# Kernel tuning notes

Measured on AMD Instinct MI355X. Metric: run time of the kernel, lower is better.

The kernel has to match this reference:

```python
import jax, jax.numpy as jnp
import numpy as np

N, D, H, K, E = 50000, 128, 4, 20, 1600000
DH = D // H
EPS = 1e-5

def _ln(x, g, b):
    m = x.mean(-1, keepdims=True)
    v = x.var(-1, keepdims=True)
    return (x - m) / jnp.sqrt(v + EPS) * g + b

def _mha(q_in, kv, in_w, in_b, out_w, out_b):
    # q_in: [N,1,D], kv: [N,K,D]; PyTorch nn.MultiheadAttention math (eval mode)
    wq, wk, wv = jnp.split(in_w, 3, axis=0)
    bq, bk, bv = jnp.split(in_b, 3, axis=0)
    n, kk, _ = kv.shape
    q = (q_in @ wq.T + bq).reshape(n, 1, H, DH)
    k = (kv @ wk.T + bk).reshape(n, kk, H, DH)
    v = (kv @ wv.T + bv).reshape(n, kk, H, DH)
    s = jnp.einsum('nqhd,nkhd->nhqk', q, k) / jnp.sqrt(jnp.asarray(DH, q.dtype))
    a = jax.nn.softmax(s, axis=-1)
    o = jnp.einsum('nhqk,nkhd->nqhd', a, v).reshape(n, 1, D)
    return o @ out_w.T + out_b

def setup_inputs() -> dict:
    key = jax.random.key(0)
    ks = jax.random.split(key, 12)
    s = 0.02
    return {
        'x': jax.random.normal(ks[0], (N, D), jnp.float32),
        'attention_samples': jax.random.randint(ks[1], (N, K), 0, N),
        'edge_src': jax.random.randint(ks[2], (E,), 0, N),
        'edge_dst': jax.random.randint(ks[3], (E,), 0, N),
        't_in_w': jax.random.normal(ks[4], (3, 3 * D, D), jnp.float32) * s,
        't_in_b': jnp.zeros((3, 3 * D), jnp.float32),
        't_out_w': jax.random.normal(ks[5], (3, D, D), jnp.float32) * s,
        't_out_b': jnp.zeros((3, D), jnp.float32),
        't_ffn_w1': jax.random.normal(ks[6], (3, 4 * D, D), jnp.float32) * s,
        't_ffn_b1': jnp.zeros((3, 4 * D), jnp.float32),
        't_ffn_w2': jax.random.normal(ks[7], (3, D, 4 * D), jnp.float32) * s,
        't_ffn_b2': jnp.zeros((3, D), jnp.float32),
        't_ln1_g': jnp.ones((3, D), jnp.float32),
        't_ln1_b': jnp.zeros((3, D), jnp.float32),
        't_ln2_g': jnp.ones((3, D), jnp.float32),
        't_ln2_b': jnp.zeros((3, D), jnp.float32),
        'g_w': jax.random.normal(ks[8], (2, D, 2 * D), jnp.float32) * s,
        'g_b': jnp.zeros((2, D), jnp.float32),
        'g_ln_g': jnp.ones((2, D), jnp.float32),
        'g_ln_b': jnp.zeros((2, D), jnp.float32),
    }

def reference(x, attention_samples, edge_src, edge_dst,
              t_in_w, t_in_b, t_out_w, t_out_b,
              t_ffn_w1, t_ffn_b1, t_ffn_w2, t_ffn_b2,
              t_ln1_g, t_ln1_b, t_ln2_g, t_ln2_b,
              g_w, g_b, g_ln_g, g_ln_b):
    def trans(h, i):
        kv = h[attention_samples]                      # [N,K,D] irregular gather
        attn = _mha(h[:, None, :], kv, t_in_w[i], t_in_b[i], t_out_w[i], t_out_b[i])[:, 0, :]
        h = _ln(h + attn, t_ln1_g[i], t_ln1_b[i])
        f = jax.nn.relu(h @ t_ffn_w1[i].T + t_ffn_b1[i]) @ t_ffn_w2[i].T + t_ffn_b2[i]
        return _ln(h + f, t_ln2_g[i], t_ln2_b[i])
    def gnn(h, i):
        neigh = jax.ops.segment_sum(h[edge_dst], edge_src, num_segments=N)  # spmm(adj, h)
        comb = jnp.concatenate([h, neigh], axis=-1)
        hn = jax.nn.relu(comb @ g_w[i].T + g_b[i])
        return _ln(hn + h, g_ln_g[i], g_ln_b[i])
    # Trans1 -> GNN1 -> Trans2 -> GNN2 -> Trans3
    x = trans(x, 0)
    x = gnn(x, 0)
    x = trans(x, 1)
    x = gnn(x, 1)
    x = trans(x, 2)
    return x
```

## Files before the change

kernel.cpp:

```cpp
#include <hip/hip_runtime.h>

#define DM 128
#define KS 20
#define BW 512
#define BSH 9
#define MAXB 128
#define HP 264

typedef __attribute__((ext_vector_type(8))) short short8;
typedef __attribute__((ext_vector_type(4))) float f32x4;
typedef __attribute__((ext_vector_type(2))) float f32x2;
typedef __attribute__((ext_vector_type(2))) __bf16 bf16x2;

__device__ __forceinline__ unsigned short f2b(float f) {
    unsigned u = __float_as_uint(f);
    u += 0x7fff + ((u >> 16) & 1);
    return (unsigned short)(u >> 16);
}
__device__ __forceinline__ float b2f(unsigned short b) {
    return __uint_as_float(((unsigned)b) << 16);
}
__device__ __forceinline__ float blo(unsigned u) { return __uint_as_float(u << 16); }
__device__ __forceinline__ float bhi(unsigned u) { return __uint_as_float(u & 0xffff0000u); }
__device__ __forceinline__ unsigned pk(float a, float b) {
    return (unsigned)f2b(a) | ((unsigned)f2b(b) << 16);
}

#if __has_builtin(__builtin_amdgcn_fdot2_f32_bf16)
__device__ __forceinline__ float dot2bf(unsigned a, unsigned b, float acc) {
    return __builtin_amdgcn_fdot2_f32_bf16(
        __builtin_bit_cast(bf16x2, a), __builtin_bit_cast(bf16x2, b), acc, false);
}
#else
__device__ __forceinline__ float dot2bf(unsigned a, unsigned b, float acc) {
    return acc + blo(a) * blo(b) + bhi(a) * bhi(b);
}
#endif

__device__ __forceinline__ float f8dec_sw(unsigned char b) {
    const int s = b >> 7, e = (b >> 3) & 15, m = b & 7;
    float v = e ? ldexpf((float)(8 + m), e - 10) : ldexpf((float)m, -9);
    return s ? -v : v;
}
template <bool HI>
__device__ __forceinline__ f32x2 fp8x2(unsigned u) {
#if __has_builtin(__builtin_amdgcn_cvt_pk_f32_fp8)
    return __builtin_amdgcn_cvt_pk_f32_fp8(u, HI);
#else
    const unsigned w = HI ? (u >> 16) : (u & 0xffffu);
    return (f32x2){f8dec_sw((unsigned char)(w & 0xff)),
                   f8dec_sw((unsigned char)(w >> 8))};
#endif
}
__device__ __forceinline__ unsigned char f8enc(float v) {
#if __has_builtin(__builtin_amdgcn_cvt_pk_fp8_f32)
    return (unsigned char)(__builtin_amdgcn_cvt_pk_fp8_f32(v, v, 0, false) & 0xff);
#else
    unsigned u = __float_as_uint(v);
    unsigned s = (u >> 24) & 0x80;
    unsigned a = u & 0x7fffffffu;
    if (a >= 0x43e00000u) return (unsigned char)(s | 0x7e);
    if (a < 0x3c000000u) {
        int r = (int)(__uint_as_float(a) * 512.f + 0.5f);
        if (r > 7) return (unsigned char)(s | 0x08);
        return (unsigned char)(s | (unsigned)r);
    }
    unsigned r = a + 0x7ffffu + ((a >> 20) & 1);
    unsigned e = (r >> 23) - 120;
    unsigned m = (r >> 20) & 7;
    return (unsigned char)(s | (e << 3) | m);
#endif
}

__global__ __launch_bounds__(256) void xcvt_kernel(
    const float* __restrict__ x, float* __restrict__ h,
    unsigned short* __restrict__ hb, int n)
{
    const int i = (blockIdx.x * 256 + threadIdx.x) * 4;
    if (i < n) {
        const float4 v = *(const float4*)(x + i);
        *(float4*)(h + i) = v;
        ((unsigned*)hb)[i / 2]     = pk(v.x, v.y);
        ((unsigned*)hb)[i / 2 + 1] = pk(v.z, v.w);
    }
}

__global__ __launch_bounds__(256) void setup_kernel(
    const float* __restrict__ t_in_w,  const float* __restrict__ t_out_w,
    const float* __restrict__ t_ffn_w1, const float* __restrict__ t_ffn_w2,
    const float* __restrict__ g_w, unsigned short* __restrict__ wbuf,
    unsigned* __restrict__ WoP, int* __restrict__ bcnt)
{
    const int tid = blockIdx.x * 256 + threadIdx.x;
    if (tid < 163840) {
        const int i4 = tid * 4;
        const float* src; int rel;
        if      (i4 < 147456) { src = t_in_w;   rel = i4; }
        else if (i4 < 196608) { src = t_out_w;  rel = i4 - 147456; }
        else if (i4 < 393216) { src = t_ffn_w1; rel = i4 - 196608; }
        else if (i4 < 589824) { src = t_ffn_w2; rel = i4 - 393216; }
        else                  { src = g_w;      rel = i4 - 589824; }
        const float4 v = *(const float4*)(src + rel);
        ((unsigned*)wbuf)[i4 / 2]     = pk(v.x, v.y);
        ((unsigned*)wbuf)[i4 / 2 + 1] = pk(v.z, v.w);
    } else if (tid < 163840 + 24576) {
        const int t2 = tid - 163840;
        const int i = t2 / 8192, rem = t2 % 8192;
        const int plane = rem >> 12, r2 = rem & 4095;
        const int k2 = r2 >> 6, j = r2 & 63;
        const int col = j + plane * 64;
        const float* W = t_out_w + (size_t)i * 16384;
        WoP[(size_t)i * 8192 + plane * 4096 + k2 * 64 + j] =
            pk(W[col * 128 + 2 * k2], W[col * 128 + 2 * k2 + 1]);
    } else if (tid < 163840 + 24576 + MAXB) {
        bcnt[tid - 163840 - 24576] = 0;
    }
}

__global__ __launch_bounds__(256) void gemm_qkv(
    const unsigned short* __restrict__ X,
    const unsigned short* __restrict__ W, const float* __restrict__ bias,
    unsigned short* __restrict__ Qbf, unsigned char* __restrict__ kv8, int M)
{
    const int tid  = threadIdx.x;
    const int wave = tid >> 6;
    const int lane = tid & 63;
    const int m0 = blockIdx.x * 128 + (wave >> 1) * 64;
    const int c0 = blockIdx.y * 64 + (wave & 1) * 32;
    const int lrow = lane & 15;
    const int quad = lane >> 4;

    f32x4 acc[4][2];
    #pragma unroll
    for (int i = 0; i < 4; ++i)
        #pragma unroll
        for (int j = 0; j < 2; ++j)
            acc[i][j] = (f32x4){0.f, 0.f, 0.f, 0.f};

    int rr[4]; bool vv[4];
    #pragma unroll
    for (int i = 0; i < 4; ++i) { rr[i] = m0 + i * 16 + lrow; vv[i] = rr[i] < M; }

    #pragma unroll
    for (int k0 = 0; k0 < 128; k0 += 32) {
        const int ko = k0 + quad * 8;
        short8 a[4];
        #pragma unroll
        for (int i = 0; i < 4; ++i) {
            a[i] = short8{};
            if (vv[i]) a[i] = *(const short8*)(X + (size_t)rr[i] * 128 + ko);
        }
        const short8 b0 = *(const short8*)(W + (size_t)(c0 + lrow) * 128 + ko);
        const short8 b1 = *(const short8*)(W + (size_t)(c0 + 16 + lrow) * 128 + ko);
        #pragma unroll
        for (int i = 0; i < 4; ++i) {
            acc[i][0] = __builtin_amdgcn_mfma_f32_16x16x32_bf16(a[i], b0, acc[i][0], 0, 0, 0);
            acc[i][1] = __builtin_amdgcn_mfma_f32_16x16x32_bf16(a[i], b1, acc[i][1], 0, 0, 0);
        }
    }

    const bool isQ = (c0 < 128);
    #pragma unroll
    for (int i = 0; i < 4; ++i) {
        const int rb = m0 + i * 16 + quad * 4;
        #pragma unroll
        for (int j = 0; j < 2; ++j) {
            const int col = c0 + j * 16 + lrow;
            const float bsv = bias[col];
            #pragma unroll
            for (int r = 0; r < 4; ++r) {
                const int row = rb + r;
                if (row < M) {
                    const float v = acc[i][j][r] + bsv;
                    if (isQ) Qbf[(size_t)row * 128 + col] = f2b(v);
                    else     kv8[(size_t)row * 256 + (col - 128)] = f8enc(v);
                }
            }
        }
    }
}

template <int CI, bool RELU, int SPLIT>
__global__ __launch_bounds__(256) void gemm_ln(
    const unsigned short* __restrict__ X0, const unsigned short* __restrict__ X1,
    const unsigned short* __restrict__ W, const float* __restrict__ bias,
    const float* __restrict__ resid,
    const float* __restrict__ g, const float* __restrict__ be,
    float* __restrict__ hF, unsigned short* __restrict__ hB, int M)
{
    __shared__ float psum[64][2][2];
    __shared__ float stats[64][2];

    const int tid  = threadIdx.x;
    const int wave = tid >> 6;
    const int lane = tid & 63;
    const int wr = (wave >> 1) * 32;
    const int wc = wave & 1;
    const int m0 = blockIdx.x * 64 + wr;
    const int c0 = wc * 64;
    const int lrow = lane & 15;
    const int quad = lane >> 4;

    f32x4 acc[2][4];
    #pragma unroll
    for (int i = 0; i < 2; ++i)
        #pragma unroll
        for (int j = 0; j < 4; ++j)
            acc[i][j] = (f32x4){0.f, 0.f, 0.f, 0.f};

    const int r0 = m0 + lrow;
    const int r1 = m0 + 16 + lrow;
    const bool v0 = r0 < M, v1 = r1 < M;

    for (int k0 = 0; k0 < CI; k0 += 32) {
        const unsigned short* xs;
        int kk, stride;
        if (SPLIT > 0 && k0 >= SPLIT) { xs = X1; kk = k0 - SPLIT; stride = CI - SPLIT; }
        else                          { xs = X0; kk = k0;         stride = (SPLIT > 0) ? SPLIT : CI; }
        const int ko = kk + quad * 8;
        short8 a0 = {}, a1 = {};
        if (v0) a0 = *(const short8*)(xs + (size_t)r0 * stride + ko);
        if (v1) a1 = *(const short8*)(xs + (size_t)r1 * stride + ko);
        const int kw = k0 + quad * 8;
        #pragma unroll
        for (int j = 0; j < 4; ++j) {
            const short8 bf = *(const short8*)(W + (size_t)(c0 + j * 16 + lrow) * CI + kw);
            acc[0][j] = __builtin_amdgcn_mfma_f32_16x16x32_bf16(a0, bf, acc[0][j], 0, 0, 0);
            acc[1][j] = __builtin_amdgcn_mfma_f32_16x16x32_bf16(a1, bf, acc[1][j], 0, 0, 0);
        }
    }

    float bcol[4], gcol[4], bec[4];
    #pragma unroll
    for (int j = 0; j < 4; ++j) {
        const int col = c0 + j * 16 + lrow;
        bcol[j] = bias[col];
        gcol[j] = g[col];
        bec[j]  = be[col];
    }

    float vals[2][4][4];
    #pragma unroll
    for (int i = 0; i < 2; ++i) {
        #pragma unroll
        for (int r = 0; r < 4; ++r) {
            const int lrel = wr + i * 16 + quad * 4 + r;
            const int row = blockIdx.x * 64 + lrel;
            const bool vr = row < M;
            float s = 0.f, s2 = 0.f;
            #pragma unroll
            for (int j = 0; j < 4; ++j) {
                const int col = c0 + j * 16 + lrow;
                float v = acc[i][j][r] + bcol[j];
                if (RELU) v = fmaxf(v, 0.f);
                if (vr) v += resid[(size_t)row * 128 + col];
                vals[i][j][r] = v;
                s += v; s2 += v * v;
            }
            s  += __shfl_xor(s, 1);  s  += __shfl_xor(s, 2);
            s  += __shfl_xor(s, 4);  s  += __shfl_xor(s, 8);
            s2 += __shfl_xor(s2, 1); s2 += __shfl_xor(s2, 2);
            s2 += __shfl_xor(s2, 4); s2 += __shfl_xor(s2, 8);
            if (lrow == 0) { psum[lrel][wc][0] = s; psum[lrel][wc][1] = s2; }
        }
    }
    __syncthreads();
    if (tid < 64) {
        const float sum   = psum[tid][0][0] + psum[tid][1][0];
        const float sumsq = psum[tid][0][1] + psum[tid][1][1];
        const float mean = sum * (1.f / 128.f);
        const float var  = sumsq * (1.f / 128.f) - mean * mean;
        stats[tid][0] = mean;
        stats[tid][1] = rsqrtf(var + 1e-5f);
    }
    __syncthreads();

    #pragma unroll
    for (int i = 0; i < 2; ++i) {
        #pragma unroll
        for (int r = 0; r < 4; ++r) {
            const int lrel = wr + i * 16 + quad * 4 + r;
            const int row = blockIdx.x * 64 + lrel;
            if (row < M) {
                const float mean = stats[lrel][0];
                const float rstd = stats[lrel][1];
                #pragma unroll
                for (int j = 0; j < 4; ++j) {
                    const int col = c0 + j * 16 + lrow;
                    const float o = (vals[i][j][r] - mean) * rstd * gcol[j] + bec[j];
                    hF[(size_t)row * 128 + col] = o;
                    hB[(size_t)row * 128 + col] = f2b(o);
                }
            }
        }
    }
}

__global__ __launch_bounds__(256, 4) void ffn_fused(
    const unsigned short* __restrict__ X,
    const unsigned short* __restrict__ W1,
    const float* __restrict__ b1,
    const unsigned short* __restrict__ W2,
    const float* __restrict__ b2,
    const float* __restrict__ resid,
    const float* __restrict__ g, const float* __restrict__ be,
    float* __restrict__ hF, unsigned short* __restrict__ hB, int M)
{
    __shared__ unsigned short Hs[32 * HP];
    __shared__ float psum[32][4][2];
    __shared__ float stats[32][2];

    const int tid  = threadIdx.x;
    const int wave = tid >> 6;
    const int lane = tid & 63;
    const int lrow = lane & 15;
    const int quad = lane >> 4;
    const int m0 = blockIdx.x * 32;

    const int c0 = wave * 32;

    const int r0 = m0 + lrow;
    const int r1 = m0 + 16 + lrow;
    const bool v0 = r0 < M, v1 = r1 < M;

    short8 xa[4], xb[4];
    #pragma unroll
    for (int k = 0; k < 4; ++k) {
        const int ko = k * 32 + quad * 8;
        xa[k] = short8{}; xb[k] = short8{};
        if (v0) xa[k] = *(const short8*)(X + (size_t)r0 * 128 + ko);
        if (v1) xb[k] = *(const short8*)(X + (size_t)r1 * 128 + ko);
    }

    float res[2][4][2];
    #pragma unroll
    for (int i = 0; i < 2; ++i)
        #pragma unroll
        for (int r = 0; r < 4; ++r) {
            const int row = m0 + i * 16 + quad * 4 + r;
            const bool vr = row < M;
            #pragma unroll
            for (int j = 0; j < 2; ++j)
                res[i][r][j] = vr ? resid[(size_t)row * 128 + c0 + j * 16 + lrow] : 0.f;
        }

    f32x4 acc2[2][2];
    #pragma unroll
    for (int i = 0; i < 2; ++i)
        #pragma unroll
        for (int j = 0; j < 2; ++j)
            acc2[i][j] = (f32x4){0.f, 0.f, 0.f, 0.f};

    #pragma unroll
    for (int chunk = 0; chunk < 2; ++chunk) {
        const int cb = chunk * 256 + wave * 64;
        const int lcb = wave * 64;
        {
            f32x4 acc[2][4];
            #pragma unroll
            for (int i = 0; i < 2; ++i)
                #pragma unroll
                for (int j = 0; j < 4; ++j)
                    acc[i][j] = (f32x4){0.f, 0.f, 0.f, 0.f};

            #pragma unroll
            for (int k = 0; k < 4; ++k) {
                const int ko = k * 32 + quad * 8;
                #pragma unroll
                for (int j = 0; j < 4; ++j) {
                    const short8 bf = *(const short8*)(W1 + (size_t)(cb + j * 16 + lrow) * 128 + ko);
                    acc[0][j] = __builtin_amdgcn_mfma_f32_16x16x32_bf16(xa[k], bf, acc[0][j], 0, 0, 0);
                    acc[1][j] = __builtin_amdgcn_mfma_f32_16x16x32_bf16(xb[k], bf, acc[1][j], 0, 0, 0);
                }
            }
            float bc[4];
            #pragma unroll
            for (int j = 0; j < 4; ++j) bc[j] = b1[cb + j * 16 + lrow];
            #pragma unroll
            for (int i = 0; i < 2; ++i) {
                #pragma unroll
                for (int r = 0; r < 4; ++r) {
                    const int lrel = i * 16 + quad * 4 + r;
                    #pragma unroll
                    for (int j = 0; j < 4; ++j)
                        Hs[lrel * HP + lcb + j * 16 + lrow] =
                            f2b(fmaxf(acc[i][j][r] + bc[j], 0.f));
                }
            }
        }
        __syncthreads();

        #pragma unroll
        for (int k0 = 0; k0 < 256; k0 += 32) {
            const int ko = k0 + quad * 8;
            const int kw = chunk * 256 + ko;
            const short8 a0 = *(const short8*)&Hs[lrow * HP + ko];
            const short8 a1 = *(const short8*)&Hs[(16 + lrow) * HP + ko];
            #pragma unroll
            for (int j = 0; j < 2; ++j) {
                const short8 bf = *(const short8*)(W2 + (size_t)(c0 + j * 16 + lrow) * 512 + kw);
                acc2[0][j] = __builtin_amdgcn_mfma_f32_16x16x32_bf16(a0, bf, acc2[0][j], 0, 0, 0);
                acc2[1][j] = __builtin_amdgcn_mfma_f32_16x16x32_bf16(a1, bf, acc2[1][j], 0, 0, 0);
            }
        }
        __syncthreads();
    }

    float bcol[2], gcol[2], bec[2];
    #pragma unroll
    for (int j = 0; j < 2; ++j) {
        const int col = c0 + j * 16 + lrow;
        bcol[j] = b2[col];
        gcol[j] = g[col];
        bec[j]  = be[col];
    }

    float vals[2][2][4];
    #pragma unroll
    for (int i = 0; i < 2; ++i) {
        #pragma unroll
        for (int r = 0; r < 4; ++r) {
            const int lrel = i * 16 + quad * 4 + r;
            const int row = m0 + lrel;
            float s = 0.f, s2 = 0.f;
            #pragma unroll
            for (int j = 0; j < 2; ++j) {
                float v = acc2[i][j][r] + bcol[j] + res[i][r][j];
                vals[i][j][r] = v;
                s += v; s2 += v * v;
            }
            s  += __shfl_xor(s, 1);  s  += __shfl_xor(s, 2);
            s  += __shfl_xor(s, 4);  s  += __shfl_xor(s, 8);
            s2 += __shfl_xor(s2, 1); s2 += __shfl_xor(s2, 2);
            s2 += __shfl_xor(s2, 4); s2 += __shfl_xor(s2, 8);
            if (lrow == 0) { psum[lrel][wave][0] = s; psum[lrel][wave][1] = s2; }
        }
    }
    __syncthreads();
    if (tid < 32) {
        const float sum   = psum[tid][0][0] + psum[tid][1][0] + psum[tid][2][0] + psum[tid][3][0];
        const float sumsq = psum[tid][0][1] + psum[tid][1][1] + psum[tid][2][1] + psum[tid][3][1];
        const float mean = sum * (1.f / 128.f);
        const float var  = sumsq * (1.f / 128.f) - mean * mean;
        stats[tid][0] = mean;
        stats[tid][1] = rsqrtf(var + 1e-5f);
    }
    __syncthreads();

    #pragma unroll
    for (int i = 0; i < 2; ++i) {
        #pragma unroll
        for (int r = 0; r < 4; ++r) {
            const int lrel = i * 16 + quad * 4 + r;
            const int row = m0 + lrel;
            if (row < M) {
                const float mean = stats[lrel][0];
                const float rstd = stats[lrel][1];
                #pragma unroll
                for (int j = 0; j < 2; ++j) {
                    const int col = c0 + j * 16 + lrow;
                    const float o = (vals[i][j][r] - mean) * rstd * gcol[j] + bec[j];
                    hF[(size_t)row * 128 + col] = o;
                    hB[(size_t)row * 128 + col] = f2b(o);
                }
            }
        }
    }
}

__global__ __launch_bounds__(256) void attn_fused(
    const unsigned short* __restrict__ qbf,
    const unsigned char* __restrict__ kv8,
    const int* __restrict__ samples,
    const unsigned* __restrict__ WoP,
    const float* __restrict__ bo,
    const float* __restrict__ g, const float* __restrict__ be,
    float* __restrict__ hF, unsigned short* __restrict__ hB, int n)
{
    __shared__ unsigned ctxs[4][64];
    const int wv = threadIdx.x >> 6;
    const int lane = threadIdx.x & 63;
    const int node0 = blockIdx.x * 4 + wv;
    const bool live = node0 < n;
    const int node = live ? node0 : (n - 1);
    const int s4 = lane >> 4;
    const int p  = lane & 15;
    const float scale = 0.17677669529663687f;

    const size_t base = (size_t)node * 128;
    const float res0 = hF[base + lane];
    const float res1 = hF[base + lane + 64];

    const uint4 qu = *(const uint4*)(qbf + (size_t)node * 128 + p * 8);

    int rows[5];
    #pragma unroll
    for (int jj = 0; jj < 5; ++jj)
        rows[jj] = samples[node * KS + jj * 4 + s4];

    uint2 kus[5], vus[5];
    #pragma unroll
    for (int jj = 0; jj < 5; ++jj) {
        const unsigned char* rb = kv8 + (size_t)rows[jj] * 256 + p * 8;
        kus[jj] = *(const uint2*)rb;
        vus[jj] = *(const uint2*)(rb + 128);
    }

    const float q0 = blo(qu.x), q1 = bhi(qu.x), q2 = blo(qu.y), q3 = bhi(qu.y);
    const float q4 = blo(qu.z), q5 = bhi(qu.z), q6 = blo(qu.w), q7 = bhi(qu.w);

    float sc[5];
    #pragma unroll
    for (int jj = 0; jj < 5; ++jj) {
        const f32x2 k0 = fp8x2<false>(kus[jj].x);
        const f32x2 k1 = fp8x2<true >(kus[jj].x);
        const f32x2 k2 = fp8x2<false>(kus[jj].y);
        const f32x2 k3 = fp8x2<true >(kus[jj].y);
        float d = q0 * k0.x;
        d = fmaf(q1, k0.y, d); d = fmaf(q2, k1.x, d); d = fmaf(q3, k1.y, d);
        d = fmaf(q4, k2.x, d); d = fmaf(q5, k2.y, d);
        d = fmaf(q6, k3.x, d); d = fmaf(q7, k3.y, d);
        d += __shfl_xor(d, 1);
        d += __shfl_xor(d, 2);
        sc[jj] = d * scale;
    }

    float m = sc[0];
    #pragma unroll
    for (int jj = 1; jj < 5; ++jj) m = fmaxf(m, sc[jj]);
    m = fmaxf(m, __shfl_xor(m, 16));
    m = fmaxf(m, __shfl_xor(m, 32));

    float l = 0.f;
    float o[8] = {};
    #pragma unroll
    for (int jj = 0; jj < 5; ++jj) {
        const float e = __expf(sc[jj] - m);
        l += e;
        const f32x2 v0 = fp8x2<false>(vus[jj].x);
        const f32x2 v1 = fp8x2<true >(vus[jj].x);
        const f32x2 v2 = fp8x2<false>(vus[jj].y);
        const f32x2 v3 = fp8x2<true >(vus[jj].y);
        o[0] = fmaf(e, v0.x, o[0]); o[1] = fmaf(e, v0.y, o[1]);
        o[2] = fmaf(e, v1.x, o[2]); o[3] = fmaf(e, v1.y, o[3]);
        o[4] = fmaf(e, v2.x, o[4]); o[5] = fmaf(e, v2.y, o[5]);
        o[6] = fmaf(e, v3.x, o[6]); o[7] = fmaf(e, v3.y, o[7]);
    }

    l += __shfl_xor(l, 16); l += __shfl_xor(l, 32);
    #pragma unroll
    for (int i = 0; i < 8; ++i) {
        o[i] += __shfl_xor(o[i], 16);
        o[i] += __shfl_xor(o[i], 32);
    }

    const float inv = 1.f / l;
    if (s4 == 0) {
        #pragma unroll
        for (int i = 0; i < 4; ++i)
            ctxs[wv][p * 4 + i] = pk(o[2 * i] * inv, o[2 * i + 1] * inv);
    }
    __syncthreads();

    const unsigned* Wa = WoP;
    const unsigned* Wb = WoP + 4096;
    float a0 = 0.f, a1 = 0.f;
    #pragma unroll 8
    for (int k2 = 0; k2 < 64; ++k2) {
        const unsigned c = ctxs[wv][k2];
        a0 = dot2bf(Wa[k2 * 64 + lane], c, a0);
        a1 = dot2bf(Wb[k2 * 64 + lane], c, a1);
    }

    float v0 = a0 + bo[lane]      + res0;
    float v1 = a1 + bo[lane + 64] + res1;
    float s = v0 + v1;
    #pragma unroll
    for (int mm = 32; mm >= 1; mm >>= 1) s += __shfl_xor(s, mm, 64);
    const float mean = s * (1.f / 128.f);
    const float d0 = v0 - mean, d1 = v1 - mean;
    float vs = d0 * d0 + d1 * d1;
    #pragma unroll
    for (int mm = 32; mm >= 1; mm >>= 1) vs += __shfl_xor(vs, mm, 64);
    const float rstd = rsqrtf(vs * (1.f / 128.f) + 1e-5f);
    if (live) {
        const float o0 = d0 * rstd * g[lane]      + be[lane];
        const float o1 = d1 * rstd * g[lane + 64] + be[lane + 64];
        hF[base + lane]      = o0;      hF[base + lane + 64] = o1;
        hB[base + lane]      = f2b(o0); hB[base + lane + 64] = f2b(o1);
    }
}

__global__ __launch_bounds__(256) void aggregate_kernel(
    const unsigned short* __restrict__ hb, const int* __restrict__ offs,
    const int* __restrict__ csr, unsigned short* __restrict__ outp, int n, int E)
{
    const int node = blockIdx.x * 4 + (threadIdx.x >> 6);
    const int lane = threadIdx.x & 63;
    if (node >= n) return;
    const int e4 = lane >> 4;
    const int p  = lane & 15;
    const int s = offs[node];
    const int e = (node == n - 1) ? E : offs[node + 1];
    float a[8] = {};
    int i = s + e4;
    for (; i + 12 < e; i += 16) {
        const int d0 = csr[i], d1 = csr[i + 4], d2 = csr[i + 8], d3 = csr[i + 12];
        const uint4 u0 = *(const uint4*)(hb + (size_t)d0 * 128 + p * 8);
        const uint4 u1 = *(const uint4*)(hb + (size_t)d1 * 128 + p * 8);
        const uint4 u2 = *(const uint4*)(hb + (size_t)d2 * 128 + p * 8);
        const uint4 u3 = *(const uint4*)(hb + (size_t)d3 * 128 + p * 8);
        a[0] += blo(u0.x) + blo(u1.x) + blo(u2.x) + blo(u3.x);
        a[1] += bhi(u0.x) + bhi(u1.x) + bhi(u2.x) + bhi(u3.x);
        a[2] += blo(u0.y) + blo(u1.y) + blo(u2.y) + blo(u3.y);
        a[3] += bhi(u0.y) + bhi(u1.y) + bhi(u2.y) + bhi(u3.y);
        a[4] += blo(u0.z) + blo(u1.z) + blo(u2.z) + blo(u3.z);
        a[5] += bhi(u0.z) + bhi(u1.z) + bhi(u2.z) + bhi(u3.z);
        a[6] += blo(u0.w) + blo(u1.w) + blo(u2.w) + blo(u3.w);
        a[7] += bhi(u0.w) + bhi(u1.w) + bhi(u2.w) + bhi(u3.w);
    }
    for (; i < e; i += 4) {
        const uint4 u = *(const uint4*)(hb + (size_t)csr[i] * 128 + p * 8);
        a[0] += blo(u.x); a[1] += bhi(u.x);
        a[2] += blo(u.y); a[3] += bhi(u.y);
        a[4] += blo(u.z); a[5] += bhi(u.z);
        a[6] += blo(u.w); a[7] += bhi(u.w);
    }
    #pragma unroll
    for (int k = 0; k < 8; ++k) {
        a[k] += __shfl_xor(a[k], 16);
        a[k] += __shfl_xor(a[k], 32);
    }
    if (e4 == 0) {
        uint4 ow;
        ow.x = pk(a[0], a[1]); ow.y = pk(a[2], a[3]);
        ow.z = pk(a[4], a[5]); ow.w = pk(a[6], a[7]);
        *(uint4*)(outp + (size_t)node * 128 + p * 8) = ow;
    }
}

__global__ __launch_bounds__(256) void bcount_kernel(
    const int* __restrict__ esrc, int* __restrict__ bcnt, int E)
{
    __shared__ int hist[MAXB];
    for (int i = threadIdx.x; i < MAXB; i += 256) hist[i] = 0;
    __syncthreads();
    const int stride = gridDim.x * 256;
    for (int e = blockIdx.x * 256 + threadIdx.x; e < E; e += stride)
        atomicAdd(&hist[esrc[e] >> BSH], 1);
    __syncthreads();
    for (int i = threadIdx.x; i < MAXB; i += 256)
        if (hist[i]) atomicAdd(&bcnt[i], hist[i]);
}

__global__ void bscan_kernel(const int* __restrict__ bcnt, int* __restrict__ boffs,
                             int* __restrict__ bcur, int NB)
{
    if (threadIdx.x == 0 && blockIdx.x == 0) {
        int run = 0;
        for (int i = 0; i < NB; ++i) { boffs[i] = run; bcur[i] = run; run += bcnt[i]; }
        boffs[NB] = run;
    }
}

__global__ __launch_bounds__(256) void bscatter_kernel(
    const int* __restrict__ esrc, const int* __restrict__ edst,
    int* __restrict__ bcur, uint2* __restrict__ ebuck, int E)
{
    __shared__ int hist[MAXB], scanb[MAXB], lstart[MAXB], gbase[MAXB], cnt2[MAXB];
    __shared__ uint2 stage[2048];
    __shared__ int gaddr[2048];
    const int t = threadIdx.x;
    const int base = blockIdx.x * 2048;
    const int nchunk = min(2048, E - base);
    for (int i = t; i < MAXB; i += 256) { hist[i] = 0; cnt2[i] = 0; }
    __syncthreads();

    int es[8], ed[8], eb[8];
    #pragma unroll
    for (int i = 0; i < 8; ++i) {
        const int idx = base + i * 256 + t;
        if (idx < E) {
            es[i] = esrc[idx]; ed[i] = edst[idx];
            eb[i] = es[i] >> BSH;
            atomicAdd(&hist[eb[i]], 1);
        } else eb[i] = -1;
    }
    __syncthreads();

    if (t < MAXB) scanb[t] = hist[t];
    __syncthreads();
    for (int off = 1; off < MAXB; off <<= 1) {
        int v = 0;
        if (t < MAXB && t >= off) v = scanb[t - off];
        __syncthreads();
        if (t < MAXB) scanb[t] += v;
        __syncthreads();
    }
    if (t < MAXB) {
        lstart[t] = scanb[t] - hist[t];
        if (hist[t] > 0) gbase[t] = atomicAdd(&bcur[t], hist[t]);
    }
    __syncthreads();

    #pragma unroll
    for (int i = 0; i < 8; ++i) {
        if (eb[i] >= 0) {
            const int li = atomicAdd(&cnt2[eb[i]], 1);
            const int pos = lstart[eb[i]] + li;
            stage[pos] = make_uint2((unsigned)es[i], (unsigned)ed[i]);
            gaddr[pos] = gbase[eb[i]] + li;
        }
    }
    __syncthreads();
    for (int i = t; i < nchunk; i += 256)
        ebuck[gaddr[i]] = stage[i];
}

__global__ __launch_bounds__(256) void bbuild_kernel(
    const uint2* __restrict__ ebuck, const int* __restrict__ bcnt,
    const int* __restrict__ boffs, int* __restrict__ offs, int* __restrict__ csr, int N)
{
    __shared__ int degl[BW], sbuf[BW], curl[BW];
    const int b = blockIdx.x;
    const int t = threadIdx.x;
    const int nbase = b * BW;
    const int nn = min(BW, N - nbase);
    const int estart = boffs[b];
    const int ecnt = bcnt[b];

    for (int i = t; i < BW; i += 256) { degl[i] = 0; curl[i] = 0; }
    __syncthreads();
    for (int i = t; i < ecnt; i += 256)
        atomicAdd(&degl[(int)ebuck[estart + i].x - nbase], 1);
    __syncthreads();

    sbuf[t] = degl[t]; sbuf[t + 256] = degl[t + 256];
    __syncthreads();
    for (int off = 1; off < BW; off <<= 1) {
        const int i1 = t + 256;
        int v0 = (t  >= off) ? sbuf[t  - off] : 0;
        int v1 = (i1 >= off) ? sbuf[i1 - off] : 0;
        __syncthreads();
        sbuf[t] += v0; sbuf[i1] += v1;
        __syncthreads();
    }
    {
        const int e0 = sbuf[t] - degl[t];
        const int e1 = sbuf[t + 256] - degl[t + 256];
        sbuf[t] = e0; sbuf[t + 256] = e1;
        if (t < nn)       offs[nbase + t]       = estart + e0;
        if (t + 256 < nn) offs[nbase + t + 256] = estart + e1;
    }
    __syncthreads();
    for (int i = t; i < ecnt; i += 256) {
        const uint2 pr = ebuck[estart + i];
        const int s = (int)pr.x - nbase;
        const int pos = estart + sbuf[s] + atomicAdd(&curl[s], 1);
        csr[pos] = (int)pr.y;
    }
}

extern "C" void kernel_launch(void* const* d_in, const int* in_sizes, int n_in,
                              void* d_out, int out_size, void* d_ws, size_t ws_size,
                              hipStream_t stream)
{
    const float* x        = (const float*)d_in[0];
    const int*   samples  = (const int*)d_in[1];
    const int*   esrc     = (const int*)d_in[2];
    const int*   edst     = (const int*)d_in[3];
    const float* t_in_w   = (const float*)d_in[4];
    const float* t_in_b   = (const float*)d_in[5];
    const float* t_out_w  = (const float*)d_in[6];
    const float* t_out_b  = (const float*)d_in[7];
    const float* t_ffn_w1 = (const float*)d_in[8];
    const float* t_ffn_b1 = (const float*)d_in[9];
    const float* t_ffn_w2 = (const float*)d_in[10];
    const float* t_ffn_b2 = (const float*)d_in[11];
    const float* t_ln1_g  = (const float*)d_in[12];
    const float* t_ln1_b  = (const float*)d_in[13];
    const float* t_ln2_g  = (const float*)d_in[14];
    const float* t_ln2_b  = (const float*)d_in[15];
    const float* g_w      = (const float*)d_in[16];
    const float* g_b      = (const float*)d_in[17];
    const float* g_ln_g   = (const float*)d_in[18];
    const float* g_ln_b   = (const float*)d_in[19];

    const int N = in_sizes[0] / DM;
    const int E = in_sizes[2];
    const int NB = (N + BW - 1) >> BSH;

    float* h = (float*)d_out;

    unsigned short* wbuf = (unsigned short*)d_ws;
    unsigned short* w_in  = wbuf;
    unsigned short* w_out = w_in  + 147456;
    unsigned short* w_f1  = w_out + 49152;
    unsigned short* w_f2  = w_f1  + 196608;
    unsigned short* w_g   = w_f2  + 196608;
    unsigned* WoP = (unsigned*)(w_g + 65536);
    unsigned short* hb  = (unsigned short*)(WoP + 3 * 8192);
    unsigned short* Bbf = hb  + (size_t)N * 128;
    unsigned short* Qbf = Bbf + (size_t)N * 128;
    unsigned char*  kv8 = (unsigned char*)(Qbf + (size_t)N * 128);
    uint2* ebuck = (uint2*)(kv8 + (size_t)N * 256);
    int* offs = (int*)(ebuck + E);
    int* csr  = offs + N;
    int* bcnt  = csr + E;
    int* boffs = bcnt + MAXB;
    int* bcur  = boffs + MAXB + 1;

    const int mt  = (N + 63) / 64;
    const int mt2 = (N + 127) / 128;
    const int mtf = (N + 31) / 32;
    const dim3 blk(256);

    xcvt_kernel<<<((N * DM) / 4 + 255) / 256, blk, 0, stream>>>(x, h, hb, N * DM);
    setup_kernel<<<(163840 + 24576 + MAXB + 255) / 256, blk, 0, stream>>>(
        t_in_w, t_out_w, t_ffn_w1, t_ffn_w2, g_w, wbuf, WoP, bcnt);

    bcount_kernel<<<(E + 2047) / 2048, blk, 0, stream>>>(esrc, bcnt, E);
    bscan_kernel<<<1, 64, 0, stream>>>(bcnt, boffs, bcur, NB);
    bscatter_kernel<<<(E + 2047) / 2048, blk, 0, stream>>>(esrc, edst, bcur, ebuck, E);
    bbuild_kernel<<<NB, blk, 0, stream>>>(ebuck, bcnt, boffs, offs, csr, N);

    const int pn_grid = (N + 3) / 4;

    for (int layer = 0; layer < 5; ++layer) {
        if (layer == 1 || layer == 3) {
            const int i = (layer == 1) ? 0 : 1;
            aggregate_kernel<<<pn_grid, blk, 0, stream>>>(hb, offs, csr, Bbf, N, E);
            gemm_ln<256, true, 128><<<mt, blk, 0, stream>>>(
                hb, Bbf, w_g + (size_t)i * 32768, g_b + i * 128, h,
                g_ln_g + i * 128, g_ln_b + i * 128, h, hb, N);
        } else {
            const int i = (layer == 0) ? 0 : (layer == 2 ? 1 : 2);
            gemm_qkv<<<dim3(mt2, 6), blk, 0, stream>>>(
                hb, w_in + (size_t)i * 49152, t_in_b + i * 384, Qbf, kv8, N);
            attn_fused<<<pn_grid, blk, 0, stream>>>(
                Qbf, kv8, samples, WoP + (size_t)i * 8192, t_out_b + i * 128,
                t_ln1_g + i * 128, t_ln1_b + i * 128, h, hb, N);
            ffn_fused<<<mtf, blk, 0, stream>>>(
                hb, w_f1 + (size_t)i * 65536, t_ffn_b1 + i * 512,
                w_f2 + (size_t)i * 65536, t_ffn_b2 + i * 128, h,
                t_ln2_g + i * 128, t_ln2_b + i * 128, h, hb, N);
        }
    }
}
```

Before: 948.1 us.

## Use MFMA for attention output projection with block-level layernorm

After: 1.010 ms. 1.07x slower.

```diff
diff --git a/kernel.cpp b/kernel.cpp
--- a/kernel.cpp
+++ b/kernel.cpp
@@ -472,12 +472,14 @@
     const unsigned short* __restrict__ qbf,
     const unsigned char* __restrict__ kv8,
     const int* __restrict__ samples,
-    const unsigned* __restrict__ WoP,
+    const unsigned short* __restrict__ Wo,
     const float* __restrict__ bo,
     const float* __restrict__ g, const float* __restrict__ be,
     float* __restrict__ hF, unsigned short* __restrict__ hB, int n)
 {
     __shared__ unsigned ctxs[4][64];
+    __shared__ float psum[4][4][2];
+    __shared__ float stats[4][2];
     const int wv = threadIdx.x >> 6;
     const int lane = threadIdx.x & 63;
     const int node0 = blockIdx.x * 4 + wv;
@@ -486,10 +488,6 @@
     const int s4 = lane >> 4;
     const int p  = lane & 15;
     const float scale = 0.17677669529663687f;
-
-    const size_t base = (size_t)node * 128;
-    const float res0 = hF[base + lane];
-    const float res1 = hF[base + lane + 64];
 
     const uint4 qu = *(const uint4*)(qbf + (size_t)node * 128 + p * 8);
 
@@ -562,32 +560,75 @@
     }
     __syncthreads();
 
-    const unsigned* Wa = WoP;
-    const unsigned* Wb = WoP + 4096;
-    float a0 = 0.f, a1 = 0.f;
-    #pragma unroll 8
-    for (int k2 = 0; k2 < 64; ++k2) {
-        const unsigned c = ctxs[wv][k2];
-        a0 = dot2bf(Wa[k2 * 64 + lane], c, a0);
-        a1 = dot2bf(Wb[k2 * 64 + lane], c, a1);
-    }
-
-    float v0 = a0 + bo[lane]      + res0;
-    float v1 = a1 + bo[lane + 64] + res1;
-    float s = v0 + v1;
-    #pragma unroll
-    for (int mm = 32; mm >= 1; mm >>= 1) s += __shfl_xor(s, mm, 64);
-    const float mean = s * (1.f / 128.f);
-    const float d0 = v0 - mean, d1 = v1 - mean;
-    float vs = d0 * d0 + d1 * d1;
-    #pragma unroll
-    for (int mm = 32; mm >= 1; mm >>= 1) vs += __shfl_xor(vs, mm, 64);
-    const float rstd = rsqrtf(vs * (1.f / 128.f) + 1e-5f);
-    if (live) {
-        const float o0 = d0 * rstd * g[lane]      + be[lane];
-        const float o1 = d1 * rstd * g[lane + 64] + be[lane + 64];
-        hF[base + lane]      = o0;      hF[base + lane + 64] = o1;
-        hB[base + lane]      = f2b(o0); hB[base + lane + 64] = f2b(o1);
+    const int lrow = p;
+    const int quad = s4;
+    f32x4 acc[2];
+    acc[0] = (f32x4){0.f, 0.f, 0.f, 0.f};
+    acc[1] = (f32x4){0.f, 0.f, 0.f, 0.f};
+    #pragma unroll
+    for (int kt = 0; kt < 4; ++kt) {
+        const uint4 av = *(const uint4*)&ctxs[lrow & 3][kt * 16 + quad * 4];
+        const short8 af = __builtin_bit_cast(short8, av);
+        #pragma unroll
+        for (int j = 0; j < 2; ++j) {
+            const int cb = wv * 32 + j * 16;
+            const short8 bf = *(const short8*)(Wo + (size_t)(cb + lrow) * 128 + kt * 32 + quad * 8);
+            acc[j] = __builtin_amdgcn_mfma_f32_16x16x32_bf16(af, bf, acc[j], 0, 0, 0);
+        }
+    }
+
+    float vals[4][2];
+    if (quad == 0) {
+        #pragma unroll
+        for (int j = 0; j < 2; ++j) {
+            const int col = wv * 32 + j * 16 + lrow;
+            const float bv = bo[col];
+            #pragma unroll
+            for (int r = 0; r < 4; ++r) {
+                const int nd = blockIdx.x * 4 + r;
+                float v = acc[j][r] + bv;
+                if (nd < n) v += hF[(size_t)nd * 128 + col];
+                vals[r][j] = v;
+            }
+        }
+        #pragma unroll
+        for (int r = 0; r < 4; ++r) {
+            float s  = vals[r][0] + vals[r][1];
+            float s2 = vals[r][0] * vals[r][0] + vals[r][1] * vals[r][1];
+            s  += __shfl_xor(s, 1);  s  += __shfl_xor(s, 2);
+            s  += __shfl_xor(s, 4);  s  += __shfl_xor(s, 8);
+            s2 += __shfl_xor(s2, 1); s2 += __shfl_xor(s2, 2);
+            s2 += __shfl_xor(s2, 4); s2 += __shfl_xor(s2, 8);
+            if (lrow == 0) { psum[r][wv][0] = s; psum[r][wv][1] = s2; }
+        }
+    }
+    __syncthreads();
+    if (threadIdx.x < 4) {
+        const int r = threadIdx.x;
+        const float sum   = psum[r][0][0] + psum[r][1][0] + psum[r][2][0] + psum[r][3][0];
+        const float sumsq = psum[r][0][1] + psum[r][1][1] + psum[r][2][1] + psum[r][3][1];
+        const float mean = sum * (1.f / 128.f);
+        const float var  = sumsq * (1.f / 128.f) - mean * mean;
+        stats[r][0] = mean;
+        stats[r][1] = rsqrtf(var + 1e-5f);
+    }
+    __syncthreads();
+    if (quad == 0) {
+        #pragma unroll
+        for (int r = 0; r < 4; ++r) {
+            const int nd = blockIdx.x * 4 + r;
+            if (nd < n) {
+                const float mean = stats[r][0];
+                const float rstd = stats[r][1];
+                #pragma unroll
+                for (int j = 0; j < 2; ++j) {
+                    const int col = wv * 32 + j * 16 + lrow;
+                    const float ov = (vals[r][j] - mean) * rstd * g[col] + be[col];
+                    hF[(size_t)nd * 128 + col] = ov;
+                    hB[(size_t)nd * 128 + col] = f2b(ov);
+                }
+            }
+        }
     }
 }
 
@@ -838,7 +879,7 @@
             gemm_qkv<<<dim3(mt2, 6), blk, 0, stream>>>(
                 hb, w_in + (size_t)i * 49152, t_in_b + i * 384, Qbf, kv8, N);
             attn_fused<<<pn_grid, blk, 0, stream>>>(
-                Qbf, kv8, samples, WoP + (size_t)i * 8192, t_out_b + i * 128,
+                Qbf, kv8, samples, w_out + (size_t)i * 16384, t_out_b + i * 128,
                 t_ln1_g + i * 128, t_ln1_b + i * 128, h, hb, N);
             ffn_fused<<<mtf, blk, 0, stream>>>(
                 hb, w_f1 + (size_t)i * 65536, t_ffn_b1 + i * 512,
```

## Use MFMA for attention output projection and single-pass FFN hidden staging

Applied to the files above, without the earlier changes.

Result: slower. 1.007 ms (+6.2%).

```diff
diff --git a/kernel.cpp b/kernel.cpp
--- a/kernel.cpp
+++ b/kernel.cpp
@@ -5,7 +5,8 @@
 #define BW 512
 #define BSH 9
 #define MAXB 128
-#define HP 264
+#define HP 520
+#define WOS 136
 
 typedef __attribute__((ext_vector_type(8))) short short8;
 typedef __attribute__((ext_vector_type(4))) float f32x4;
@@ -344,6 +345,43 @@
                 res[i][r][j] = vr ? resid[(size_t)row * 128 + c0 + j * 16 + lrow] : 0.f;
         }
 
+    #pragma unroll
+    for (int half = 0; half < 2; ++half) {
+        const int cb = half * 256 + wave * 64;
+        f32x4 acc[2][4];
+        #pragma unroll
+        for (int i = 0; i < 2; ++i)
+            #pragma unroll
+            for (int j = 0; j < 4; ++j)
+                acc[i][j] = (f32x4){0.f, 0.f, 0.f, 0.f};
+
+        #pragma unroll
+        for (int k = 0; k < 4; ++k) {
+            const int ko = k * 32 + quad * 8;
+            #pragma unroll
+            for (int j = 0; j < 4; ++j) {
+                const short8 bf = *(const short8*)(W1 + (size_t)(cb + j * 16 + lrow) * 128 + ko);
+                acc[0][j] = __builtin_amdgcn_mfma_f32_16x16x32_bf16(xa[k], bf, acc[0][j], 0, 0, 0);
+                acc[1][j] = __builtin_amdgcn_mfma_f32_16x16x32_bf16(xb[k], bf, acc[1][j], 0, 0, 0);
+            }
+        }
+        float bc[4];
+        #pragma unroll
+        for (int j = 0; j < 4; ++j) bc[j] = b1[cb + j * 16 + lrow];
+        #pragma unroll
+        for (int i = 0; i < 2; ++i) {
+            #pragma unroll
+            for (int r = 0; r < 4; ++r) {
+                const int lrel = i * 16 + quad * 4 + r;
+                #pragma unroll
+                for (int j = 0; j < 4; ++j)
+                    Hs[lrel * HP + cb + j * 16 + lrow] =
+                        f2b(fmaxf(acc[i][j][r] + bc[j], 0.f));
+            }
+        }
+    }
+    __syncthreads();
+
     f32x4 acc2[2][2];
     #pragma unroll
     for (int i = 0; i < 2; ++i)
@@ -352,58 +390,16 @@
             acc2[i][j] = (f32x4){0.f, 0.f, 0.f, 0.f};
 
     #pragma unroll
-    for (int chunk = 0; chunk < 2; ++chunk) {
-        const int cb = chunk * 256 + wave * 64;
-        const int lcb = wave * 64;
-        {
-            f32x4 acc[2][4];
-            #pragma unroll
-            for (int i = 0; i < 2; ++i)
-                #pragma unroll
-                for (int j = 0; j < 4; ++j)
-                    acc[i][j] = (f32x4){0.f, 0.f, 0.f, 0.f};
-
-            #pragma unroll
-            for (int k = 0; k < 4; ++k) {
-                const int ko = k * 32 + quad * 8;
-                #pragma unroll
-                for (int j = 0; j < 4; ++j) {
-                    const short8 bf = *(const short8*)(W1 + (size_t)(cb + j * 16 + lrow) * 128 + ko);
-                    acc[0][j] = __builtin_amdgcn_mfma_f32_16x16x32_bf16(xa[k], bf, acc[0][j], 0, 0, 0);
-                    acc[1][j] = __builtin_amdgcn_mfma_f32_16x16x32_bf16(xb[k], bf, acc[1][j], 0, 0, 0);
-                }
-            }
-            float bc[4];
-            #pragma unroll
-            for (int j = 0; j < 4; ++j) bc[j] = b1[cb + j * 16 + lrow];
-            #pragma unroll
-            for (int i = 0; i < 2; ++i) {
-                #pragma unroll
-                for (int r = 0; r < 4; ++r) {
-                    const int lrel = i * 16 + quad * 4 + r;
-                    #pragma unroll
-                    for (int j = 0; j < 4; ++j)
-                        Hs[lrel * HP + lcb + j * 16 + lrow] =
-                            f2b(fmaxf(acc[i][j][r] + bc[j], 0.f));
-                }
-            }
-        }
-        __syncthreads();
-
-        #pragma unroll
-        for (int k0 = 0; k0 < 256; k0 += 32) {
-            const int ko = k0 + quad * 8;
-            const int kw = chunk * 256 + ko;
-            const short8 a0 = *(const short8*)&Hs[lrow * HP + ko];
-            const short8 a1 = *(const short8*)&Hs[(16 + lrow) * HP + ko];
-            #pragma unroll
-            for (int j = 0; j < 2; ++j) {
-                const short8 bf = *(const short8*)(W2 + (size_t)(c0 + j * 16 + lrow) * 512 + kw);
-                acc2[0][j] = __builtin_amdgcn_mfma_f32_16x16x32_bf16(a0, bf, acc2[0][j], 0, 0, 0);
-                acc2[1][j] = __builtin_amdgcn_mfma_f32_16x16x32_bf16(a1, bf, acc2[1][j], 0, 0, 0);
-            }
-        }
-        __syncthreads();
+    for (int k0 = 0; k0 < 512; k0 += 32) {
+        const int ko = k0 + quad * 8;
+        const short8 a0 = *(const short8*)&Hs[lrow * HP + ko];
+        const short8 a1 = *(const short8*)&Hs[(16 + lrow) * HP + ko];
+        #pragma unroll
+        for (int j = 0; j < 2; ++j) {
+            const short8 bf = *(const short8*)(W2 + (size_t)(c0 + j * 16 + lrow) * 512 + ko);
+            acc2[0][j] = __builtin_amdgcn_mfma_f32_16x16x32_bf16(a0, bf, acc2[0][j], 0, 0, 0);
+            acc2[1][j] = __builtin_amdgcn_mfma_f32_16x16x32_bf16(a1, bf, acc2[1][j], 0, 0, 0);
+        }
     }
 
     float bcol[2], gcol[2], bec[2];
@@ -472,14 +468,25 @@
     const unsigned short* __restrict__ qbf,
     const unsigned char* __restrict__ kv8,
     const int* __restrict__ samples,
-    const unsigned* __restrict__ WoP,
+    const unsigned short* __restrict__ Wo,
     const float* __restrict__ bo,
     const float* __restrict__ g, const float* __restrict__ be,
     float* __restrict__ hF, unsigned short* __restrict__ hB, int n)
 {
-    __shared__ unsigned ctxs[4][64];
-    const int wv = threadIdx.x >> 6;
-    const int lane = threadIdx.x & 63;
+    __shared__ unsigned short WoS[128 * WOS];
+
+    const int tid = threadIdx.x;
+    {
+        const int row = tid >> 1, half = tid & 1;
+        const uint4* src = (const uint4*)(Wo + row * 128 + half * 64);
+        uint4* dst = (uint4*)(WoS + row * WOS + half * 64);
+        #pragma unroll
+        for (int i = 0; i < 8; ++i) dst[i] = src[i];
+    }
+    __syncthreads();
+
+    const int wv = tid >> 6;
+    const int lane = tid & 63;
     const int node0 = blockIdx.x * 4 + wv;
     const bool live = node0 < n;
     const int node = live ? node0 : (n - 1);
@@ -488,8 +495,9 @@
     const float scale = 0.17677669529663687f;
 
     const size_t base = (size_t)node * 128;
-    const float res0 = hF[base + lane];
-    const float res1 = hF[base + lane + 64];
+    float res[8];
+    #pragma unroll
+    for (int j = 0; j < 8; ++j) res[j] = hF[base + j * 16 + p];
 
     const uint4 qu = *(const uint4*)(qbf + (size_t)node * 128 + p * 8);
 
@@ -555,39 +563,52 @@
     }
 
     const float inv = 1.f / l;
-    if (s4 == 0) {
-        #pragma unroll
-        for (int i = 0; i < 4; ++i)
-            ctxs[wv][p * 4 + i] = pk(o[2 * i] * inv, o[2 * i + 1] * inv);
-    }
-    __syncthreads();
-
-    const unsigned* Wa = WoP;
-    const unsigned* Wb = WoP + 4096;
-    float a0 = 0.f, a1 = 0.f;
-    #pragma unroll 8
-    for (int k2 = 0; k2 < 64; ++k2) {
-        const unsigned c = ctxs[wv][k2];
-        a0 = dot2bf(Wa[k2 * 64 + lane], c, a0);
-        a1 = dot2bf(Wb[k2 * 64 + lane], c, a1);
-    }
-
-    float v0 = a0 + bo[lane]      + res0;
-    float v1 = a1 + bo[lane + 64] + res1;
-    float s = v0 + v1;
-    #pragma unroll
-    for (int mm = 32; mm >= 1; mm >>= 1) s += __shfl_xor(s, mm, 64);
+    unsigned cw[4];
+    #pragma unroll
+    for (int i = 0; i < 4; ++i)
+        cw[i] = pk(o[2 * i] * inv, o[2 * i + 1] * inv);
+
+    f32x4 acc[8];
+    #pragma unroll
+    for (int j = 0; j < 8; ++j) acc[j] = (f32x4){0.f, 0.f, 0.f, 0.f};
+    #pragma unroll
+    for (int kt = 0; kt < 4; ++kt) {
+        const int srcl = kt * 4 + s4;
+        uint4 aw;
+        aw.x = (unsigned)__shfl((int)cw[0], srcl);
+        aw.y = (unsigned)__shfl((int)cw[1], srcl);
+        aw.z = (unsigned)__shfl((int)cw[2], srcl);
+        aw.w = (unsigned)__shfl((int)cw[3], srcl);
+        const short8 af = __builtin_bit_cast(short8, aw);
+        #pragma unroll
+        for (int j = 0; j < 8; ++j) {
+            const short8 bf = *(const short8*)&WoS[(j * 16 + p) * WOS + kt * 32 + s4 * 8];
+            acc[j] = __builtin_amdgcn_mfma_f32_16x16x32_bf16(af, bf, acc[j], 0, 0, 0);
+        }
+    }
+
+    float val[8];
+    float s = 0.f, s2 = 0.f;
+    #pragma unroll
+    for (int j = 0; j < 8; ++j) {
+        val[j] = acc[j][0] + bo[j * 16 + p] + res[j];
+        s += val[j]; s2 += val[j] * val[j];
+    }
+    s  += __shfl_xor(s, 1);  s  += __shfl_xor(s, 2);
+    s  += __shfl_xor(s, 4);  s  += __shfl_xor(s, 8);
+    s2 += __shfl_xor(s2, 1); s2 += __shfl_xor(s2, 2);
+    s2 += __shfl_xor(s2, 4); s2 += __shfl_xor(s2, 8);
     const float mean = s * (1.f / 128.f);
-    const float d0 = v0 - mean, d1 = v1 - mean;
-    float vs = d0 * d0 + d1 * d1;
-    #pragma unroll
-    for (int mm = 32; mm >= 1; mm >>= 1) vs += __shfl_xor(vs, mm, 64);
-    const float rstd = rsqrtf(vs * (1.f / 128.f) + 1e-5f);
+    const float var  = s2 * (1.f / 128.f) - mean * mean;
+    const float rstd = rsqrtf(var + 1e-5f);
+
     if (live) {
-        const float o0 = d0 * rstd * g[lane]      + be[lane];
-        const float o1 = d1 * rstd * g[lane + 64] + be[lane + 64];
-        hF[base + lane]      = o0;      hF[base + lane + 64] = o1;
-        hB[base + lane]      = f2b(o0); hB[base + lane + 64] = f2b(o1);
+        const int j0 = s4 * 2, j1 = s4 * 2 + 1;
+        const int c0 = j0 * 16 + p, c1 = j1 * 16 + p;
+        const float o0 = (val[j0] - mean) * rstd * g[c0] + be[c0];
+        const float o1 = (val[j1] - mean) * rstd * g[c1] + be[c1];
+        hF[base + c0] = o0;      hF[base + c1] = o1;
+        hB[base + c0] = f2b(o0); hB[base + c1] = f2b(o1);
     }
 }
 
@@ -838,7 +859,7 @@
             gemm_qkv<<<dim3(mt2, 6), blk, 0, stream>>>(
                 hb, w_in + (size_t)i * 49152, t_in_b + i * 384, Qbf, kv8, N);
             attn_fused<<<pn_grid, blk, 0, stream>>>(
-                Qbf, kv8, samples, WoP + (size_t)i * 8192, t_out_b + i * 128,
+                Qbf, kv8, samples, w_out + (size_t)i * 16384, t_out_b + i * 128,
                 t_ln1_g + i * 128, t_ln1_b + i * 128, h, hb, N);
             ffn_fused<<<mtf, blk, 0, stream>>>(
                 hb, w_f1 + (size_t)i * 65536, t_ffn_b1 + i * 512,
```
